# Performance work log

Hardware: AMD Instinct MI355X
Metric: run time of the kernel (lower is better)

Reference implementation:

```python
import jax, jax.numpy as jnp
import numpy as np

D_MODEL = 768
NUM_HEADS = 12
D_K = D_MODEL // NUM_HEADS


def setup_inputs() -> dict:
    key = jax.random.key(0)
    ks = jax.random.split(key, 7)
    B, T = 2, 2048
    scale = 1.0 / np.sqrt(D_MODEL)
    return {
        "query": jax.random.normal(ks[0], (B, T, D_MODEL), dtype=jnp.float32),
        "key": jax.random.normal(ks[1], (B, T, D_MODEL), dtype=jnp.float32),
        "value": jax.random.normal(ks[2], (B, T, D_MODEL), dtype=jnp.float32),
        # nn.Linear(d_model, d_model, bias=False) weights, stored [out, in] as in torch
        "W_q": jax.random.normal(ks[3], (D_MODEL, D_MODEL), dtype=jnp.float32) * scale,
        "W_k": jax.random.normal(ks[4], (D_MODEL, D_MODEL), dtype=jnp.float32) * scale,
        "W_v": jax.random.normal(ks[5], (D_MODEL, D_MODEL), dtype=jnp.float32) * scale,
        "W_o": jax.random.normal(ks[6], (D_MODEL, D_MODEL), dtype=jnp.float32) * scale,
    }


def _split_heads(x):
    # [B, T, H*Dk] -> [B, H, T, Dk]
    B, T, _ = x.shape
    return x.reshape(B, T, NUM_HEADS, D_K).transpose(0, 2, 1, 3)


def reference(query, key, value, W_q, W_k, W_v, W_o):
    # Linear projections (torch Linear: y = x @ W.T)
    Q = _split_heads(query @ W_q.T)
    K = _split_heads(key @ W_k.T)
    V = _split_heads(value @ W_v.T)

    # Naive scaled dot-product attention: full [B,H,Tq,Tk] score matrix
    scores = jnp.einsum("bhqd,bhkd->bhqk", Q, K) / jnp.sqrt(jnp.float32(D_K))
    weights = jax.nn.softmax(scores, axis=-1)
    attn = jnp.einsum("bhqk,bhkd->bhqd", weights, V)

    # [B,H,T,Dk] -> [B,T,D_model], then output projection
    B, H, T, Dk = attn.shape
    attn = attn.transpose(0, 2, 1, 3).reshape(B, T, H * Dk)
    output = attn @ W_o.T
    return output, weights
```

## Files before the change

kernel.cpp:

```cpp
#include <hip/hip_runtime.h>
#include <cstdint>

#define HD   12
#define TSEQ 2048
#define DM   768
#define DK   64
#define BATCH 2

__device__ __forceinline__ void gemm_nt_core(
    const float* __restrict__ A, const float* __restrict__ B,
    float* __restrict__ C, int m0, int n0, int K,
    int lda, int ldb, int ldc, float alpha)
{
    __shared__ float As[8][132];
    __shared__ float Bs[8][132];

    const int t = threadIdx.x;
    const int row = t & 127;
    const int kh4 = (t >> 7) * 4;
    const float* Arow = A + (size_t)(m0 + row) * lda + kh4;
    const float* Brow = B + (size_t)(n0 + row) * ldb + kh4;

    const int w  = t >> 6;
    const int l  = t & 63;
    const int orow = (w >> 1) * 64 + (l >> 3) * 8;
    const int ocol = (w & 1) * 64 + (l & 7) * 8;

    float acc[8][8];
    #pragma unroll
    for (int i = 0; i < 8; ++i)
        #pragma unroll
        for (int j = 0; j < 8; ++j) acc[i][j] = 0.f;

    for (int k0 = 0; k0 < K; k0 += 8) {
        const float4 av = *(const float4*)(Arow + k0);
        const float4 bv = *(const float4*)(Brow + k0);
        __syncthreads();
        As[kh4 + 0][row] = av.x; As[kh4 + 1][row] = av.y;
        As[kh4 + 2][row] = av.z; As[kh4 + 3][row] = av.w;
        Bs[kh4 + 0][row] = bv.x; Bs[kh4 + 1][row] = bv.y;
        Bs[kh4 + 2][row] = bv.z; Bs[kh4 + 3][row] = bv.w;
        __syncthreads();
        #pragma unroll
        for (int kk = 0; kk < 8; ++kk) {
            const float4 a0 = *(const float4*)&As[kk][orow];
            const float4 a1 = *(const float4*)&As[kk][orow + 4];
            const float4 b0 = *(const float4*)&Bs[kk][ocol];
            const float4 b1 = *(const float4*)&Bs[kk][ocol + 4];
            const float a[8] = {a0.x, a0.y, a0.z, a0.w, a1.x, a1.y, a1.z, a1.w};
            const float b[8] = {b0.x, b0.y, b0.z, b0.w, b1.x, b1.y, b1.z, b1.w};
            #pragma unroll
            for (int i = 0; i < 8; ++i)
                #pragma unroll
                for (int j = 0; j < 8; ++j)
                    acc[i][j] = fmaf(a[i], b[j], acc[i][j]);
        }
    }

    #pragma unroll
    for (int i = 0; i < 8; ++i) {
        float* crow = C + (size_t)(m0 + orow + i) * ldc + n0 + ocol;
        *(float4*)crow = make_float4(acc[i][0] * alpha, acc[i][1] * alpha,
                                     acc[i][2] * alpha, acc[i][3] * alpha);
        *(float4*)(crow + 4) = make_float4(acc[i][4] * alpha, acc[i][5] * alpha,
                                           acc[i][6] * alpha, acc[i][7] * alpha);
    }
}

__global__ __launch_bounds__(256) void gemm_qkv(
    const float* __restrict__ q, const float* __restrict__ k,
    const float* __restrict__ v,
    const float* __restrict__ Wq, const float* __restrict__ Wk,
    const float* __restrict__ Wv,
    float* __restrict__ Qp, float* __restrict__ Kp, float* __restrict__ Vp)
{
    const int by  = blockIdx.y;
    const int mat = by / 6;
    const int nb  = by % 6;
    const float* A = (mat == 0) ? q  : (mat == 1) ? k  : v;
    const float* B = (mat == 0) ? Wq : (mat == 1) ? Wk : Wv;
    float*       C = (mat == 0) ? Qp : (mat == 1) ? Kp : Vp;
    gemm_nt_core(A, B, C, blockIdx.x * 128, nb * 128, DM, DM, DM, DM, 1.f);
}

__global__ __launch_bounds__(256) void gemm_out(
    const float* __restrict__ ctx, const float* __restrict__ Wo,
    float* __restrict__ out)
{
    gemm_nt_core(ctx, Wo, out, blockIdx.x * 128, blockIdx.y * 128,
                 DM, DM, DM, DM, 1.f);
}

__global__ __launch_bounds__(256) void attn_scores(
    const float* __restrict__ Qp, const float* __restrict__ Kp,
    float* __restrict__ Wt)
{
    const int z = blockIdx.z, b = z / HD, h = z % HD;
    gemm_nt_core(Qp + (size_t)b * TSEQ * DM + h * DK,
                 Kp + (size_t)b * TSEQ * DM + h * DK,
                 Wt + (size_t)z * TSEQ * TSEQ,
                 blockIdx.x * 128, blockIdx.y * 128,
                 DK, DM, DM, TSEQ, 0.125f);
}

__global__ __launch_bounds__(256) void softmax_rows(float* __restrict__ Wt)
{
    float* p = Wt + (size_t)blockIdx.x * TSEQ;
    const int t = threadIdx.x;
    const float4 va = *(const float4*)(p + t * 4);
    const float4 vb = *(const float4*)(p + 1024 + t * 4);
    float v[8] = {va.x, va.y, va.z, va.w, vb.x, vb.y, vb.z, vb.w};

    float m = -3.4e38f;
    #pragma unroll
    for (int i = 0; i < 8; ++i) m = fmaxf(m, v[i]);
    #pragma unroll
    for (int off = 32; off > 0; off >>= 1) m = fmaxf(m, __shfl_down(m, off));
    __shared__ float redm[4];
    __shared__ float reds[4];
    const int lane = t & 63, wid = t >> 6;
    if (lane == 0) redm[wid] = m;
    __syncthreads();
    m = fmaxf(fmaxf(redm[0], redm[1]), fmaxf(redm[2], redm[3]));

    float s = 0.f;
    #pragma unroll
    for (int i = 0; i < 8; ++i) { v[i] = __expf(v[i] - m); s += v[i]; }
    #pragma unroll
    for (int off = 32; off > 0; off >>= 1) s += __shfl_down(s, off);
    if (lane == 0) reds[wid] = s;
    __syncthreads();
    s = reds[0] + reds[1] + reds[2] + reds[3];
    const float inv = 1.f / s;

    *(float4*)(p + t * 4) =
        make_float4(v[0] * inv, v[1] * inv, v[2] * inv, v[3] * inv);
    *(float4*)(p + 1024 + t * 4) =
        make_float4(v[4] * inv, v[5] * inv, v[6] * inv, v[7] * inv);
}

__global__ __launch_bounds__(256) void attn_pv(
    const float* __restrict__ Wt, const float* __restrict__ Vp,
    float* __restrict__ ctx)
{
    const int z = blockIdx.z, b = z / HD, h = z % HD;
    const float* A = Wt + (size_t)z * TSEQ * TSEQ;
    const float* V = Vp + (size_t)b * TSEQ * DM + h * DK;

    __shared__ float Ws[16][132];
    __shared__ float Vs[16][68];

    const int t = threadIdx.x;
    const int m0 = blockIdx.x * 128;
    const int arow = t & 127;
    const int kh8  = (t >> 7) * 8;
    const float* Arow = A + (size_t)(m0 + arow) * TSEQ + kh8;
    const int vr = t >> 4, vc = (t & 15) * 4;
    const float* Vrow = V + (size_t)vr * DM + vc;
    const int oty = t >> 4;
    const int otx = t & 15;

    float acc[8][4];
    #pragma unroll
    for (int i = 0; i < 8; ++i)
        #pragma unroll
        for (int j = 0; j < 4; ++j) acc[i][j] = 0.f;

    for (int k0 = 0; k0 < TSEQ; k0 += 16) {
        const float4 a0 = *(const float4*)(Arow + k0);
        const float4 a1 = *(const float4*)(Arow + k0 + 4);
        const float4 vv = *(const float4*)(Vrow + (size_t)k0 * DM);
        __syncthreads();
        Ws[kh8 + 0][arow] = a0.x; Ws[kh8 + 1][arow] = a0.y;
        Ws[kh8 + 2][arow] = a0.z; Ws[kh8 + 3][arow] = a0.w;
        Ws[kh8 + 4][arow] = a1.x; Ws[kh8 + 5][arow] = a1.y;
        Ws[kh8 + 6][arow] = a1.z; Ws[kh8 + 7][arow] = a1.w;
        *(float4*)&Vs[vr][vc] = vv;
        __syncthreads();
        #pragma unroll
        for (int kk = 0; kk < 16; ++kk) {
            const float4 a0v = *(const float4*)&Ws[kk][oty * 8];
            const float4 a1v = *(const float4*)&Ws[kk][oty * 8 + 4];
            const float4 bv  = *(const float4*)&Vs[kk][otx * 4];
            const float a[8] = {a0v.x, a0v.y, a0v.z, a0v.w,
                                a1v.x, a1v.y, a1v.z, a1v.w};
            const float bb[4] = {bv.x, bv.y, bv.z, bv.w};
            #pragma unroll
            for (int i = 0; i < 8; ++i)
                #pragma unroll
                for (int j = 0; j < 4; ++j)
                    acc[i][j] = fmaf(a[i], bb[j], acc[i][j]);
        }
    }

    float* cbase = ctx + ((size_t)b * TSEQ + m0 + oty * 8) * DM + h * DK + otx * 4;
    #pragma unroll
    for (int i = 0; i < 8; ++i)
        *(float4*)(cbase + (size_t)i * DM) =
            make_float4(acc[i][0], acc[i][1], acc[i][2], acc[i][3]);
}

extern "C" void kernel_launch(void* const* d_in, const int* in_sizes, int n_in,
                              void* d_out, int out_size, void* d_ws, size_t ws_size,
                              hipStream_t stream)
{
    const float* q  = (const float*)d_in[0];
    const float* k  = (const float*)d_in[1];
    const float* v  = (const float*)d_in[2];
    const float* Wq = (const float*)d_in[3];
    const float* Wk = (const float*)d_in[4];
    const float* Wv = (const float*)d_in[5];
    const float* Wo = (const float*)d_in[6];

    float* out = (float*)d_out;
    const int BT = BATCH * TSEQ;
    float* wts = out + (size_t)BT * DM;

    float* Qp  = (float*)d_ws;
    float* Kp  = Qp + (size_t)BT * DM;
    float* Vp  = Kp + (size_t)BT * DM;
    float* ctx = Vp + (size_t)BT * DM;

    gemm_qkv<<<dim3(BT / 128, 18), 256, 0, stream>>>(q, k, v, Wq, Wk, Wv,
                                                     Qp, Kp, Vp);
    attn_scores<<<dim3(TSEQ / 128, TSEQ / 128, BATCH * HD), 256, 0, stream>>>(
        Qp, Kp, wts);
    softmax_rows<<<BATCH * HD * TSEQ, 256, 0, stream>>>(wts);
    attn_pv<<<dim3(TSEQ / 128, 1, BATCH * HD), 256, 0, stream>>>(wts, Vp, ctx);
    gemm_out<<<dim3(BT / 128, DM / 128), 256, 0, stream>>>(ctx, Wo, out);
}
```

Before: 1.256 ms.

## Split-K attention PV with fused reduction in output GEMM, add register prefetch

```diff
diff --git a/kernel.cpp b/kernel.cpp
--- a/kernel.cpp
+++ b/kernel.cpp
@@ -7,19 +7,22 @@
 #define DK   64
 #define BATCH 2
 
+template<bool SUMA>
 __device__ __forceinline__ void gemm_nt_core(
-    const float* __restrict__ A, const float* __restrict__ B,
-    float* __restrict__ C, int m0, int n0, int K,
-    int lda, int ldb, int ldc, float alpha)
-{
-    __shared__ float As[8][132];
-    __shared__ float Bs[8][132];
+    const float* __restrict__ A, const float* __restrict__ A2,
+    const float* __restrict__ B, float* __restrict__ C,
+    int m0, int n0, int K, int lda, int ldb, int ldc, float alpha)
+{
+    __shared__ float As[16][132];
+    __shared__ float Bs[16][132];
 
     const int t = threadIdx.x;
     const int row = t & 127;
-    const int kh4 = (t >> 7) * 4;
-    const float* Arow = A + (size_t)(m0 + row) * lda + kh4;
-    const float* Brow = B + (size_t)(n0 + row) * ldb + kh4;
+    const int kh8 = (t >> 7) * 8;
+    const float* Arow = A + (size_t)(m0 + row) * lda + kh8;
+    const float* Brow = B + (size_t)(n0 + row) * ldb + kh8;
+    const float* A2row = nullptr;
+    if (SUMA) A2row = A2 + (size_t)(m0 + row) * lda + kh8;
 
     const int w  = t >> 6;
     const int l  = t & 63;
@@ -32,23 +35,46 @@
         #pragma unroll
         for (int j = 0; j < 8; ++j) acc[i][j] = 0.f;
 
-    for (int k0 = 0; k0 < K; k0 += 8) {
-        const float4 av = *(const float4*)(Arow + k0);
-        const float4 bv = *(const float4*)(Brow + k0);
-        __syncthreads();
-        As[kh4 + 0][row] = av.x; As[kh4 + 1][row] = av.y;
-        As[kh4 + 2][row] = av.z; As[kh4 + 3][row] = av.w;
-        Bs[kh4 + 0][row] = bv.x; Bs[kh4 + 1][row] = bv.y;
-        Bs[kh4 + 2][row] = bv.z; Bs[kh4 + 3][row] = bv.w;
-        __syncthreads();
-        #pragma unroll
-        for (int kk = 0; kk < 8; ++kk) {
-            const float4 a0 = *(const float4*)&As[kk][orow];
-            const float4 a1 = *(const float4*)&As[kk][orow + 4];
-            const float4 b0 = *(const float4*)&Bs[kk][ocol];
-            const float4 b1 = *(const float4*)&Bs[kk][ocol + 4];
-            const float a[8] = {a0.x, a0.y, a0.z, a0.w, a1.x, a1.y, a1.z, a1.w};
-            const float b[8] = {b0.x, b0.y, b0.z, b0.w, b1.x, b1.y, b1.z, b1.w};
+    float4 a0 = *(const float4*)(Arow);
+    float4 a1 = *(const float4*)(Arow + 4);
+    float4 b0 = *(const float4*)(Brow);
+    float4 b1 = *(const float4*)(Brow + 4);
+    float4 c0, c1;
+    if (SUMA) { c0 = *(const float4*)(A2row); c1 = *(const float4*)(A2row + 4); }
+
+    for (int k0 = 0; k0 < K; k0 += 16) {
+        __syncthreads();
+        if (SUMA) {
+            a0.x += c0.x; a0.y += c0.y; a0.z += c0.z; a0.w += c0.w;
+            a1.x += c1.x; a1.y += c1.y; a1.z += c1.z; a1.w += c1.w;
+        }
+        As[kh8 + 0][row] = a0.x; As[kh8 + 1][row] = a0.y;
+        As[kh8 + 2][row] = a0.z; As[kh8 + 3][row] = a0.w;
+        As[kh8 + 4][row] = a1.x; As[kh8 + 5][row] = a1.y;
+        As[kh8 + 6][row] = a1.z; As[kh8 + 7][row] = a1.w;
+        Bs[kh8 + 0][row] = b0.x; Bs[kh8 + 1][row] = b0.y;
+        Bs[kh8 + 2][row] = b0.z; Bs[kh8 + 3][row] = b0.w;
+        Bs[kh8 + 4][row] = b1.x; Bs[kh8 + 5][row] = b1.y;
+        Bs[kh8 + 6][row] = b1.z; Bs[kh8 + 7][row] = b1.w;
+        __syncthreads();
+        if (k0 + 16 < K) {
+            a0 = *(const float4*)(Arow + k0 + 16);
+            a1 = *(const float4*)(Arow + k0 + 20);
+            b0 = *(const float4*)(Brow + k0 + 16);
+            b1 = *(const float4*)(Brow + k0 + 20);
+            if (SUMA) {
+                c0 = *(const float4*)(A2row + k0 + 16);
+                c1 = *(const float4*)(A2row + k0 + 20);
+            }
+        }
+        #pragma unroll
+        for (int kk = 0; kk < 16; ++kk) {
+            const float4 f0 = *(const float4*)&As[kk][orow];
+            const float4 f1 = *(const float4*)&As[kk][orow + 4];
+            const float4 g0 = *(const float4*)&Bs[kk][ocol];
+            const float4 g1 = *(const float4*)&Bs[kk][ocol + 4];
+            const float a[8] = {f0.x, f0.y, f0.z, f0.w, f1.x, f1.y, f1.z, f1.w};
+            const float b[8] = {g0.x, g0.y, g0.z, g0.w, g1.x, g1.y, g1.z, g1.w};
             #pragma unroll
             for (int i = 0; i < 8; ++i)
                 #pragma unroll
@@ -80,15 +106,17 @@
     const float* A = (mat == 0) ? q  : (mat == 1) ? k  : v;
     const float* B = (mat == 0) ? Wq : (mat == 1) ? Wk : Wv;
     float*       C = (mat == 0) ? Qp : (mat == 1) ? Kp : Vp;
-    gemm_nt_core(A, B, C, blockIdx.x * 128, nb * 128, DM, DM, DM, DM, 1.f);
-}
-
+    gemm_nt_core<false>(A, nullptr, B, C, blockIdx.x * 128, nb * 128,
+                        DM, DM, DM, DM, 1.f);
+}
+
+template<bool SUMA>
 __global__ __launch_bounds__(256) void gemm_out(
-    const float* __restrict__ ctx, const float* __restrict__ Wo,
-    float* __restrict__ out)
-{
-    gemm_nt_core(ctx, Wo, out, blockIdx.x * 128, blockIdx.y * 128,
-                 DM, DM, DM, DM, 1.f);
+    const float* __restrict__ ctx0, const float* __restrict__ ctx1,
+    const float* __restrict__ Wo, float* __restrict__ out)
+{
+    gemm_nt_core<SUMA>(ctx0, ctx1, Wo, out, blockIdx.x * 128, blockIdx.y * 128,
+                       DM, DM, DM, DM, 1.f);
 }
 
 __global__ __launch_bounds__(256) void attn_scores(
@@ -96,11 +124,11 @@
     float* __restrict__ Wt)
 {
     const int z = blockIdx.z, b = z / HD, h = z % HD;
-    gemm_nt_core(Qp + (size_t)b * TSEQ * DM + h * DK,
-                 Kp + (size_t)b * TSEQ * DM + h * DK,
-                 Wt + (size_t)z * TSEQ * TSEQ,
-                 blockIdx.x * 128, blockIdx.y * 128,
-                 DK, DM, DM, TSEQ, 0.125f);
+    gemm_nt_core<false>(Qp + (size_t)b * TSEQ * DM + h * DK, nullptr,
+                        Kp + (size_t)b * TSEQ * DM + h * DK,
+                        Wt + (size_t)z * TSEQ * TSEQ,
+                        blockIdx.x * 128, blockIdx.y * 128,
+                        DK, DM, DM, TSEQ, 0.125f);
 }
 
 __global__ __launch_bounds__(256) void softmax_rows(float* __restrict__ Wt)
@@ -141,11 +169,13 @@
 
 __global__ __launch_bounds__(256) void attn_pv(
     const float* __restrict__ Wt, const float* __restrict__ Vp,
-    float* __restrict__ ctx)
+    float* __restrict__ ctxp, int kchunk)
 {
     const int z = blockIdx.z, b = z / HD, h = z % HD;
-    const float* A = Wt + (size_t)z * TSEQ * TSEQ;
-    const float* V = Vp + (size_t)b * TSEQ * DM + h * DK;
+    const int kbase = blockIdx.y * kchunk;
+    float* ctx = ctxp + (size_t)blockIdx.y * (size_t)BATCH * TSEQ * DM;
+    const float* A = Wt + (size_t)z * TSEQ * TSEQ + kbase;
+    const float* V = Vp + ((size_t)b * TSEQ + kbase) * DM + h * DK;
 
     __shared__ float Ws[16][132];
     __shared__ float Vs[16][68];
@@ -166,10 +196,11 @@
         #pragma unroll
         for (int j = 0; j < 4; ++j) acc[i][j] = 0.f;
 
-    for (int k0 = 0; k0 < TSEQ; k0 += 16) {
-        const float4 a0 = *(const float4*)(Arow + k0);
-        const float4 a1 = *(const float4*)(Arow + k0 + 4);
-        const float4 vv = *(const float4*)(Vrow + (size_t)k0 * DM);
+    float4 a0 = *(const float4*)(Arow);
+    float4 a1 = *(const float4*)(Arow + 4);
+    float4 vv = *(const float4*)(Vrow);
+
+    for (int k0 = 0; k0 < kchunk; k0 += 16) {
         __syncthreads();
         Ws[kh8 + 0][arow] = a0.x; Ws[kh8 + 1][arow] = a0.y;
         Ws[kh8 + 2][arow] = a0.z; Ws[kh8 + 3][arow] = a0.w;
@@ -177,6 +208,11 @@
         Ws[kh8 + 6][arow] = a1.z; Ws[kh8 + 7][arow] = a1.w;
         *(float4*)&Vs[vr][vc] = vv;
         __syncthreads();
+        if (k0 + 16 < kchunk) {
+            a0 = *(const float4*)(Arow + k0 + 16);
+            a1 = *(const float4*)(Arow + k0 + 20);
+            vv = *(const float4*)(Vrow + (size_t)(k0 + 16) * DM);
+        }
         #pragma unroll
         for (int kk = 0; kk < 16; ++kk) {
             const float4 a0v = *(const float4*)&Ws[kk][oty * 8];
@@ -216,16 +252,25 @@
     const int BT = BATCH * TSEQ;
     float* wts = out + (size_t)BT * DM;
 
-    float* Qp  = (float*)d_ws;
-    float* Kp  = Qp + (size_t)BT * DM;
-    float* Vp  = Kp + (size_t)BT * DM;
-    float* ctx = Vp + (size_t)BT * DM;
+    const size_t bufE = (size_t)BT * DM;
+    float* Qp   = (float*)d_ws;
+    float* Kp   = Qp + bufE;
+    float* Vp   = Kp + bufE;
+    float* ctx0 = Vp + bufE;
+    float* ctx1 = ctx0 + bufE;
+    const int nsplit = (ws_size >= 5 * bufE * sizeof(float)) ? 2 : 1;
 
     gemm_qkv<<<dim3(BT / 128, 18), 256, 0, stream>>>(q, k, v, Wq, Wk, Wv,
                                                      Qp, Kp, Vp);
     attn_scores<<<dim3(TSEQ / 128, TSEQ / 128, BATCH * HD), 256, 0, stream>>>(
         Qp, Kp, wts);
     softmax_rows<<<BATCH * HD * TSEQ, 256, 0, stream>>>(wts);
-    attn_pv<<<dim3(TSEQ / 128, 1, BATCH * HD), 256, 0, stream>>>(wts, Vp, ctx);
-    gemm_out<<<dim3(BT / 128, DM / 128), 256, 0, stream>>>(ctx, Wo, out);
-}
+    attn_pv<<<dim3(TSEQ / 128, nsplit, BATCH * HD), 256, 0, stream>>>(
+        wts, Vp, ctx0, TSEQ / nsplit);
+    if (nsplit == 2)
+        gemm_out<true><<<dim3(BT / 128, DM / 128), 256, 0, stream>>>(
+            ctx0, ctx1, Wo, out);
+    else
+        gemm_out<false><<<dim3(BT / 128, DM / 128), 256, 0, stream>>>(
+            ctx0, nullptr, Wo, out);
+}
```

Result: faster. 1.196 ms (-4.8%).
